# Kernel optimization log

Measured on AMD Instinct MI355X. Metric: run time of the kernel, lower is better.

Reference implementation:

```python
import jax, jax.numpy as jnp
import numpy as np

N = 512      # hidden states
M = 32000    # observation vocab
B = 64       # batch
TMAX = 256   # max sequence length


def setup_inputs() -> dict:
    key = jax.random.key(0)
    k1, k2, k3, k4, k5 = jax.random.split(key, 5)
    return {
        "x": jax.random.randint(k1, (B, TMAX), 0, M),          # observations
        "T": jax.random.randint(k2, (B,), 1, TMAX + 1),        # lengths in [1, TMAX]
        "trans": jax.random.normal(k3, (N, N), dtype=jnp.float32),  # unnormalized transition
        "emis": jax.random.normal(k4, (N, M), dtype=jnp.float32),   # unnormalized emission
        "prior": jax.random.normal(k5, (N,), dtype=jnp.float32),    # unnormalized state priors
    }


def reference(x, T, trans, emis, prior):
    # columns of transition matrix sum to 1 (log_softmax over dim=0 in torch)
    log_A = jax.nn.log_softmax(trans, axis=0)    # (N, N): log_A[j, k] = log p(z_t=j | z_{t-1}=k)
    log_E = jax.nn.log_softmax(emis, axis=1)     # (N, M)
    log_pi = jax.nn.log_softmax(prior, axis=0)   # (N,)

    # emission log-probs for every timestep, gathered once: (B, TMAX, N)
    em = log_E.T[x]

    alpha0 = em[:, 0, :] + log_pi                # (B, N)

    def step(alpha, em_t):
        # out[b, j] = em_t[b, j] + logsumexp_k (log_A[j, k] + alpha[b, k])
        new = em_t + jax.nn.logsumexp(alpha[:, None, :] + log_A[None, :, :], axis=2)
        return new, new

    _, alphas = jax.lax.scan(step, alpha0, jnp.swapaxes(em[:, 1:, :], 0, 1))  # (TMAX-1, B, N)
    log_alpha = jnp.concatenate([alpha0[:, None, :], jnp.swapaxes(alphas, 0, 1)], axis=1)  # (B, TMAX, N)

    log_sums = jax.nn.logsumexp(log_alpha, axis=2)                       # (B, TMAX)
    log_probs = jnp.take_along_axis(log_sums, (T - 1)[:, None], axis=1)  # (B, 1)
    return log_probs
```

## Files before the change

kernel.cpp:

```cpp
#include <hip/hip_runtime.h>
#include <math.h>

#define Nn 512
#define Mm 32000
#define Bb 64
#define Tt 256
#define NCONS 4
#define NPROD 128

typedef float v4f __attribute__((ext_vector_type(4)));
typedef float f4  __attribute__((ext_vector_type(4)));
typedef int   v4i __attribute__((ext_vector_type(4)));
typedef int   v8i __attribute__((ext_vector_type(8)));

__device__ inline int pk4fp8(float a, float b, float c, float d) {
  int r = __builtin_amdgcn_cvt_pk_fp8_f32(a, b, 0, false);
  r = __builtin_amdgcn_cvt_pk_fp8_f32(c, d, r, true);
  return r;
}

__global__ void k_colsum(const float* __restrict__ trans, float* __restrict__ colsum) {
  int tid = threadIdx.x;
  int j0 = blockIdx.x * 16;
  float a0 = 0.f, a1 = 0.f;
  for (int r = 0; r < 16; ++r) {
    a0 += __expf(trans[(j0 + r) * Nn + tid]);
    a1 += __expf(trans[(j0 + r) * Nn + 256 + tid]);
  }
  atomicAdd(&colsum[tid], a0);
  atomicAdd(&colsum[256 + tid], a1);
}

__global__ void k_writeA8(const float* __restrict__ trans, const float* __restrict__ colsum,
                          int* __restrict__ A8) {
  int d = blockIdx.x * 256 + threadIdx.x;
  int j = d >> 7, k0 = (d & 127) << 2;
  float v0 = 256.f * __expf(trans[j * Nn + k0 + 0]) / colsum[k0 + 0];
  float v1 = 256.f * __expf(trans[j * Nn + k0 + 1]) / colsum[k0 + 1];
  float v2 = 256.f * __expf(trans[j * Nn + k0 + 2]) / colsum[k0 + 2];
  float v3 = 256.f * __expf(trans[j * Nn + k0 + 3]) / colsum[k0 + 3];
  A8[d] = pk4fp8(v0, v1, v2, v3);
}

__global__ __attribute__((amdgpu_flat_work_group_size(512, 512), amdgpu_waves_per_eu(2, 2)))
void k_fused(
    const char* __restrict__ A8, const float* __restrict__ emis,
    const int* __restrict__ x, const float* __restrict__ prior,
    const int* __restrict__ Tlen, float* __restrict__ Pem2,
    int* __restrict__ progress, float* __restrict__ out)
{
  __shared__ __align__(16) char ybuf[2][16 * Nn];
  __shared__ __align__(16) float Spart[2][16][12];
  __shared__ __align__(16) float ss[512];
  __shared__ __align__(16) f4 ss4[512];
  const int tid = threadIdx.x;

  if (blockIdx.x >= NCONS) {
    const int p = blockIdx.x - NCONS;
    const int j0 = p * 4;

    float e = __expf(prior[tid]);
    ss[tid] = e; __syncthreads();
    for (int off = 256; off; off >>= 1) { if (tid < off) ss[tid] += ss[tid + off]; __syncthreads(); }
    const float ptot = ss[0];

    const f4* q0 = (const f4*)(emis + (size_t)(j0 + 0) * Mm);
    const f4* q1 = (const f4*)(emis + (size_t)(j0 + 1) * Mm);
    const f4* q2 = (const f4*)(emis + (size_t)(j0 + 2) * Mm);
    const f4* q3 = (const f4*)(emis + (size_t)(j0 + 3) * Mm);
    f4 a4 = {0.f, 0.f, 0.f, 0.f};
    for (int i = tid; i < Mm / 4; i += 512) {
      f4 v0 = q0[i], v1 = q1[i], v2 = q2[i], v3 = q3[i];
      a4[0] += (__expf(v0[0]) + __expf(v0[1])) + (__expf(v0[2]) + __expf(v0[3]));
      a4[1] += (__expf(v1[0]) + __expf(v1[1])) + (__expf(v1[2]) + __expf(v1[3]));
      a4[2] += (__expf(v2[0]) + __expf(v2[1])) + (__expf(v2[2]) + __expf(v2[3]));
      a4[3] += (__expf(v3[0]) + __expf(v3[1])) + (__expf(v3[2]) + __expf(v3[3]));
    }
    ss4[tid] = a4; __syncthreads();
    for (int off = 256; off; off >>= 1) { if (tid < off) ss4[tid] += ss4[tid + off]; __syncthreads(); }
    f4 tot = ss4[0];
    f4 rs, fz;
    #pragma unroll
    for (int q = 0; q < 4; ++q) {
      rs[q] = 32768.f / tot[q];
      fz[q] = rs[q] * 256.f * __expf(prior[j0 + q]) / ptot;
    }

    const float* r0 = emis + (size_t)(j0 + 0) * Mm;
    const float* r1 = emis + (size_t)(j0 + 1) * Mm;
    const float* r2 = emis + (size_t)(j0 + 2) * Mm;
    const float* r3 = emis + (size_t)(j0 + 3) * Mm;
    f4* P4 = (f4*)Pem2;
    for (int c8 = 0; c8 < 8; ++c8) {
      #pragma unroll
      for (int r = 0; r < 4; ++r) {
        int idx = c8 * 2048 + r * 512 + tid;
        int t = idx >> 6, b = idx & 63;
        int mv = x[b * Tt + t];
        f4 fq = (t == 0) ? fz : rs;
        f4 o = { __expf(r0[mv]) * fq[0], __expf(r1[mv]) * fq[1],
                 __expf(r2[mv]) * fq[2], __expf(r3[mv]) * fq[3] };
        P4[t * 8192 + (b >> 4) * 2048 + p * 16 + (b & 15)] = o;
      }
      __syncthreads();
      if (tid == 0) {
        __builtin_amdgcn_fence(__ATOMIC_RELEASE, "agent");
        __hip_atomic_fetch_add(&progress[c8], 1, __ATOMIC_RELAXED, __HIP_MEMORY_SCOPE_AGENT);
      }
    }
    return;
  }

  const int g = blockIdx.x;
  const int w = tid >> 6, lane = tid & 63;
  const int c = lane & 15, kq = lane >> 4;
  const int jw = w * 64;
  const int swz = (c & 7) << 4;
  const int b = g * 16 + c;

  v8i af[4][4];
  #pragma unroll
  for (int rt = 0; rt < 4; ++rt)
    #pragma unroll
    for (int kc = 0; kc < 4; ++kc)
      af[rt][kc] = *reinterpret_cast<const v8i*>(
          A8 + (size_t)(jw + rt * 16 + c) * Nn + kc * 128 + kq * 32);

  #pragma unroll
  for (int rt = 0; rt < 4; ++rt)
    #pragma unroll
    for (int kc = 0; kc < 4; ++kc)
      asm volatile("" : "+v"(af[rt][kc]));

  const int Tb = Tlen[b];
  int E = 23;
  int csafe = 0;

  #define ENSURE(NEED)                                                                      \
    while (csafe <= (NEED)) {                                                               \
      if (__hip_atomic_load(&progress[csafe], __ATOMIC_RELAXED,                             \
                            __HIP_MEMORY_SCOPE_AGENT) >= NPROD) {                           \
        ++csafe;                                                                            \
        __builtin_amdgcn_fence(__ATOMIC_ACQUIRE, "agent");                                  \
      } else __builtin_amdgcn_s_sleep(2);                                                   \
    }

  const int roA0 = (c * Nn + kq * 32) ^ swz;
  const int roB0 = roA0 ^ 16;
  const int wf0 = (c * Nn + jw + kq * 4) ^ swz;
  const int wf1 = wf0 ^ 16, wf2 = wf0 ^ 32, wf3 = wf0 ^ 48;
  char* const yb0 = &ybuf[0][0];

  const char* rdA_e = yb0 + roA0;
  const char* rdB_e = yb0 + roB0;
  const char* rdA_o = rdA_e + 8192;
  const char* rdB_o = rdB_e + 8192;
  char* const wb_o = yb0 + 8192;
  char* const wb_e = yb0;
  const float* sprd0 = &Spart[0][c][0];
  const float* sprd1 = &Spart[1][c][0];
  float* spwr0 = &Spart[1][c][w];
  float* spwr1 = &Spart[0][c][w];

  if (tid < 192) ((float*)&Spart[0][0][0])[tid] = 0.f;
  __syncthreads();

  ENSURE(0);

  {
    int cc = tid & 15, grp = tid >> 4, jb = grp * 16, sz = (cc & 7) << 4;
    const f4* P0 = (const f4*)Pem2 + g * 2048 + (jb >> 2) * 16 + cc;
    float psum = 0.f;
    #pragma unroll
    for (int q = 0; q < 4; ++q) {
      f4 v = P0[q * 16];
      psum += (v[0] + v[1]) + (v[2] + v[3]);
      *reinterpret_cast<int*>(yb0 + ((cc * Nn + jb + q * 4) ^ sz)) = pk4fp8(v[0], v[1], v[2], v[3]);
    }
    atomicAdd(&Spart[0][cc][grp & 7], psum);
  }
  __syncthreads();

  const f4* pemP = (const f4*)Pem2 + (8192 + g * 2048 + jw * 4 + kq * 16 + c);

  union BU { v8i v; v4i h[2]; };

  #define RTCHAIN(RT, BF0, BF1, BF2, BF3, PEM, WF)                                           \
    {                                                                                        \
      v4f a = {0.f, 0.f, 0.f, 0.f};                                                         \
      a = __builtin_amdgcn_mfma_scale_f32_16x16x128_f8f6f4(af[RT][0], BF0.v, a, 0,0,0, 0x7F, 0, 0x7F); \
      a = __builtin_amdgcn_mfma_scale_f32_16x16x128_f8f6f4(af[RT][1], BF1.v, a, 0,0,0, 0x7F, 0, 0x7F); \
      a = __builtin_amdgcn_mfma_scale_f32_16x16x128_f8f6f4(af[RT][2], BF2.v, a, 0,0,0, 0x7F, 0, 0x7F); \
      a = __builtin_amdgcn_mfma_scale_f32_16x16x128_f8f6f4(af[RT][3], BF3.v, a, 0,0,0, 0x7F, 0, 0x7F); \
      v4f v = a * ((PEM) * scl4);                                                            \
      *(int*)(wbase + (WF)) = pk4fp8(v[0], v[1], v[2], v[3]);                                \
      vsum += (v[0] + v[1]) + (v[2] + v[3]);                                                 \
    }

  #define STEPBODY(RDA, RDB, WBASE, SPWP)                                                    \
    {                                                                                        \
      BU b0, b1, b2, b3;                                                                     \
      b0.h[0] = *(const v4i*)((RDA) + 0);   b0.h[1] = *(const v4i*)((RDB) + 0);              \
      b1.h[0] = *(const v4i*)((RDA) + 128); b1.h[1] = *(const v4i*)((RDB) + 128);            \
      b2.h[0] = *(const v4i*)((RDA) + 256); b2.h[1] = *(const v4i*)((RDB) + 256);            \
      b3.h[0] = *(const v4i*)((RDA) + 384); b3.h[1] = *(const v4i*)((RDB) + 384);            \
      v4f scl4 = {scl, scl, scl, scl};                                                       \
      char* const wbase = (WBASE);                                                           \
      float vsum = 0.f;                                                                      \
      RTCHAIN(0, b0, b1, b2, b3, pem0, wf0)                                                  \
      RTCHAIN(1, b0, b1, b2, b3, pem1, wf1)                                                  \
      RTCHAIN(2, b0, b1, b2, b3, pem2, wf2)                                                  \
      RTCHAIN(3, b0, b1, b2, b3, pem3, wf3)                                                  \
      vsum += __shfl_xor(vsum, 16);                                                          \
      vsum += __shfl_xor(vsum, 32);                                                          \
      if (kq == 0) *(SPWP) = vsum;                                                           \
    }

  for (int t = 1; t <= Tt; t += 2) {
    {
      f4 pem0 = pemP[0], pem1 = pemP[64], pem2 = pemP[128], pem3 = pemP[192];
      f4 s0 = *(const f4*)sprd0;
      f4 s1 = *(const f4*)(sprd0 + 4);
      f4 st = s0 + s1;
      float S = (st[0] + st[1]) + (st[2] + st[3]);
      int expb = (int)((__float_as_uint(S) >> 23) & 0xFF);
      if (w == 0 && kq == 0 && Tb == t) out[b] = __logf(S) - (float)E * 0.69314718056f;
      E += 150 - expb;
      float scl = __uint_as_float((unsigned)(254 - expb) << 23);

      STEPBODY(rdA_e, rdB_e, wb_o, spwr0)
      __syncthreads();
    }
    {
      const int T = t + 1;
      if (T < Tt && (T & 31) == 0) ENSURE(T >> 5);
      f4 pem0, pem1, pem2, pem3;
      const f4* p2 = pemP + 8192;
      if (T < Tt) { pem0 = p2[0]; pem1 = p2[64]; pem2 = p2[128]; pem3 = p2[192]; }
      f4 s0 = *(const f4*)sprd1;
      f4 s1 = *(const f4*)(sprd1 + 4);
      f4 st = s0 + s1;
      float S = (st[0] + st[1]) + (st[2] + st[3]);
      int expb = (int)((__float_as_uint(S) >> 23) & 0xFF);
      if (w == 0 && kq == 0 && Tb == T) out[b] = __logf(S) - (float)E * 0.69314718056f;
      if (T == Tt) goto done;
      E += 150 - expb;
      float scl = __uint_as_float((unsigned)(254 - expb) << 23);

      STEPBODY(rdA_o, rdB_o, wb_e, spwr1)
      __syncthreads();
    }
    pemP += 16384;
  }
done: ;
  #undef RTCHAIN
  #undef STEPBODY
  #undef ENSURE
}

extern "C" void kernel_launch(void* const* d_in, const int* in_sizes, int n_in,
                              void* d_out, int out_size, void* d_ws, size_t ws_size,
                              hipStream_t stream) {
  const int*   x     = (const int*)  d_in[0];
  const int*   Tlen  = (const int*)  d_in[1];
  const float* trans = (const float*)d_in[2];
  const float* emis  = (const float*)d_in[3];
  const float* prior = (const float*)d_in[4];
  float* out = (float*)d_out;

  char* w = (char*)d_ws;
  char*  A8       = (char*)(w);
  float* colsum   = (float*)(w + (512 << 10));
  int*   progress = (int*)  (w + (512 << 10) + 4096);
  float* Pem2     = (float*)(w + (1024 << 10));

  hipMemsetAsync(w + (512 << 10), 0, 8192, stream);
  k_colsum <<<32,  256, 0, stream>>>(trans, colsum);
  k_writeA8<<<256, 256, 0, stream>>>(trans, colsum, (int*)A8);
  k_fused  <<<NCONS + NPROD, 512, 0, stream>>>(A8, emis, x, prior, Tlen, Pem2, progress, out);
}
```

Before: 346.5 us.

## Compute per-step normalizer with an all-ones MFMA instead of shared-memory partial sums

Replaces the cross-wave shared-memory reduction of each step's state sum with an extra scaled-FP8 MFMA against an all-ones A operand, so every wave gets the column sum of the current alpha directly from the matrix unit. This removes the Spart buffer, the shuffle reductions and the extra LDS traffic, and interleaves the four row-tile MFMA chains for better issue overlap. In exchange it adds four MFMAs per step and takes the normalizer from the FP8-quantized alpha, which may shift accuracy slightly.

```diff
diff --git a/kernel.cpp b/kernel.cpp
--- a/kernel.cpp
+++ b/kernel.cpp
@@ -50,7 +50,6 @@
     int* __restrict__ progress, float* __restrict__ out)
 {
   __shared__ __align__(16) char ybuf[2][16 * Nn];
-  __shared__ __align__(16) float Spart[2][16][12];
   __shared__ __align__(16) float ss[512];
   __shared__ __align__(16) f4 ss4[512];
   const int tid = threadIdx.x;
@@ -126,11 +125,16 @@
       af[rt][kc] = *reinterpret_cast<const v8i*>(
           A8 + (size_t)(jw + rt * 16 + c) * Nn + kc * 128 + kq * 32);
 
+  v8i onesv;
+  #pragma unroll
+  for (int u = 0; u < 8; ++u) onesv[u] = 0x38383838;
+
   #pragma unroll
   for (int rt = 0; rt < 4; ++rt)
     #pragma unroll
     for (int kc = 0; kc < 4; ++kc)
       asm volatile("" : "+v"(af[rt][kc]));
+  asm volatile("" : "+v"(onesv));
 
   const int Tb = Tlen[b];
   int E = 23;
@@ -157,27 +161,17 @@
   const char* rdB_o = rdB_e + 8192;
   char* const wb_o = yb0 + 8192;
   char* const wb_e = yb0;
-  const float* sprd0 = &Spart[0][c][0];
-  const float* sprd1 = &Spart[1][c][0];
-  float* spwr0 = &Spart[1][c][w];
-  float* spwr1 = &Spart[0][c][w];
-
-  if (tid < 192) ((float*)&Spart[0][0][0])[tid] = 0.f;
-  __syncthreads();
 
   ENSURE(0);
 
   {
     int cc = tid & 15, grp = tid >> 4, jb = grp * 16, sz = (cc & 7) << 4;
     const f4* P0 = (const f4*)Pem2 + g * 2048 + (jb >> 2) * 16 + cc;
-    float psum = 0.f;
     #pragma unroll
     for (int q = 0; q < 4; ++q) {
       f4 v = P0[q * 16];
-      psum += (v[0] + v[1]) + (v[2] + v[3]);
       *reinterpret_cast<int*>(yb0 + ((cc * Nn + jb + q * 4) ^ sz)) = pk4fp8(v[0], v[1], v[2], v[3]);
     }
-    atomicAdd(&Spart[0][cc][grp & 7], psum);
   }
   __syncthreads();
 
@@ -185,50 +179,59 @@
 
   union BU { v8i v; v4i h[2]; };
 
-  #define RTCHAIN(RT, BF0, BF1, BF2, BF3, PEM, WF)                                           \
+  #define LOADMFMA(RDA, RDB)                                                                 \
+    BU b0, b1, b2, b3;                                                                       \
+    b0.h[0] = *(const v4i*)((RDA) + 0);   b0.h[1] = *(const v4i*)((RDB) + 0);                \
+    b1.h[0] = *(const v4i*)((RDA) + 128); b1.h[1] = *(const v4i*)((RDB) + 128);              \
+    b2.h[0] = *(const v4i*)((RDA) + 256); b2.h[1] = *(const v4i*)((RDB) + 256);              \
+    b3.h[0] = *(const v4i*)((RDA) + 384); b3.h[1] = *(const v4i*)((RDB) + 384);              \
+    v4f a0 = {0.f,0.f,0.f,0.f}, a1 = {0.f,0.f,0.f,0.f};                                     \
+    v4f a2 = {0.f,0.f,0.f,0.f}, a3 = {0.f,0.f,0.f,0.f};                                     \
+    v4f as_ = {0.f,0.f,0.f,0.f};                                                            \
+    a0  = __builtin_amdgcn_mfma_scale_f32_16x16x128_f8f6f4(af[0][0], b0.v, a0, 0,0,0, 0x7F, 0, 0x7F); \
+    a1  = __builtin_amdgcn_mfma_scale_f32_16x16x128_f8f6f4(af[1][0], b0.v, a1, 0,0,0, 0x7F, 0, 0x7F); \
+    a2  = __builtin_amdgcn_mfma_scale_f32_16x16x128_f8f6f4(af[2][0], b0.v, a2, 0,0,0, 0x7F, 0, 0x7F); \
+    a3  = __builtin_amdgcn_mfma_scale_f32_16x16x128_f8f6f4(af[3][0], b0.v, a3, 0,0,0, 0x7F, 0, 0x7F); \
+    as_ = __builtin_amdgcn_mfma_scale_f32_16x16x128_f8f6f4(onesv,    b0.v, as_, 0,0,0, 0x7F, 0, 0x7F); \
+    a0  = __builtin_amdgcn_mfma_scale_f32_16x16x128_f8f6f4(af[0][1], b1.v, a0, 0,0,0, 0x7F, 0, 0x7F); \
+    a1  = __builtin_amdgcn_mfma_scale_f32_16x16x128_f8f6f4(af[1][1], b1.v, a1, 0,0,0, 0x7F, 0, 0x7F); \
+    a2  = __builtin_amdgcn_mfma_scale_f32_16x16x128_f8f6f4(af[2][1], b1.v, a2, 0,0,0, 0x7F, 0, 0x7F); \
+    a3  = __builtin_amdgcn_mfma_scale_f32_16x16x128_f8f6f4(af[3][1], b1.v, a3, 0,0,0, 0x7F, 0, 0x7F); \
+    as_ = __builtin_amdgcn_mfma_scale_f32_16x16x128_f8f6f4(onesv,    b1.v, as_, 0,0,0, 0x7F, 0, 0x7F); \
+    a0  = __builtin_amdgcn_mfma_scale_f32_16x16x128_f8f6f4(af[0][2], b2.v, a0, 0,0,0, 0x7F, 0, 0x7F); \
+    a1  = __builtin_amdgcn_mfma_scale_f32_16x16x128_f8f6f4(af[1][2], b2.v, a1, 0,0,0, 0x7F, 0, 0x7F); \
+    a2  = __builtin_amdgcn_mfma_scale_f32_16x16x128_f8f6f4(af[2][2], b2.v, a2, 0,0,0, 0x7F, 0, 0x7F); \
+    a3  = __builtin_amdgcn_mfma_scale_f32_16x16x128_f8f6f4(af[3][2], b2.v, a3, 0,0,0, 0x7F, 0, 0x7F); \
+    as_ = __builtin_amdgcn_mfma_scale_f32_16x16x128_f8f6f4(onesv,    b2.v, as_, 0,0,0, 0x7F, 0, 0x7F); \
+    a0  = __builtin_amdgcn_mfma_scale_f32_16x16x128_f8f6f4(af[0][3], b3.v, a0, 0,0,0, 0x7F, 0, 0x7F); \
+    a1  = __builtin_amdgcn_mfma_scale_f32_16x16x128_f8f6f4(af[1][3], b3.v, a1, 0,0,0, 0x7F, 0, 0x7F); \
+    a2  = __builtin_amdgcn_mfma_scale_f32_16x16x128_f8f6f4(af[2][3], b3.v, a2, 0,0,0, 0x7F, 0, 0x7F); \
+    a3  = __builtin_amdgcn_mfma_scale_f32_16x16x128_f8f6f4(af[3][3], b3.v, a3, 0,0,0, 0x7F, 0, 0x7F); \
+    as_ = __builtin_amdgcn_mfma_scale_f32_16x16x128_f8f6f4(onesv,    b3.v, as_, 0,0,0, 0x7F, 0, 0x7F);
+
+  #define EPILOG(WBASE)                                                                      \
     {                                                                                        \
-      v4f a = {0.f, 0.f, 0.f, 0.f};                                                         \
-      a = __builtin_amdgcn_mfma_scale_f32_16x16x128_f8f6f4(af[RT][0], BF0.v, a, 0,0,0, 0x7F, 0, 0x7F); \
-      a = __builtin_amdgcn_mfma_scale_f32_16x16x128_f8f6f4(af[RT][1], BF1.v, a, 0,0,0, 0x7F, 0, 0x7F); \
-      a = __builtin_amdgcn_mfma_scale_f32_16x16x128_f8f6f4(af[RT][2], BF2.v, a, 0,0,0, 0x7F, 0, 0x7F); \
-      a = __builtin_amdgcn_mfma_scale_f32_16x16x128_f8f6f4(af[RT][3], BF3.v, a, 0,0,0, 0x7F, 0, 0x7F); \
-      v4f v = a * ((PEM) * scl4);                                                            \
-      *(int*)(wbase + (WF)) = pk4fp8(v[0], v[1], v[2], v[3]);                                \
-      vsum += (v[0] + v[1]) + (v[2] + v[3]);                                                 \
-    }
-
-  #define STEPBODY(RDA, RDB, WBASE, SPWP)                                                    \
-    {                                                                                        \
-      BU b0, b1, b2, b3;                                                                     \
-      b0.h[0] = *(const v4i*)((RDA) + 0);   b0.h[1] = *(const v4i*)((RDB) + 0);              \
-      b1.h[0] = *(const v4i*)((RDA) + 128); b1.h[1] = *(const v4i*)((RDB) + 128);            \
-      b2.h[0] = *(const v4i*)((RDA) + 256); b2.h[1] = *(const v4i*)((RDB) + 256);            \
-      b3.h[0] = *(const v4i*)((RDA) + 384); b3.h[1] = *(const v4i*)((RDB) + 384);            \
       v4f scl4 = {scl, scl, scl, scl};                                                       \
-      char* const wbase = (WBASE);                                                           \
-      float vsum = 0.f;                                                                      \
-      RTCHAIN(0, b0, b1, b2, b3, pem0, wf0)                                                  \
-      RTCHAIN(1, b0, b1, b2, b3, pem1, wf1)                                                  \
-      RTCHAIN(2, b0, b1, b2, b3, pem2, wf2)                                                  \
-      RTCHAIN(3, b0, b1, b2, b3, pem3, wf3)                                                  \
-      vsum += __shfl_xor(vsum, 16);                                                          \
-      vsum += __shfl_xor(vsum, 32);                                                          \
-      if (kq == 0) *(SPWP) = vsum;                                                           \
+      v4f v0 = a0 * (pem0 * scl4);                                                           \
+      v4f v1 = a1 * (pem1 * scl4);                                                           \
+      v4f v2 = a2 * (pem2 * scl4);                                                           \
+      v4f v3 = a3 * (pem3 * scl4);                                                           \
+      *(int*)((WBASE) + wf0) = pk4fp8(v0[0], v0[1], v0[2], v0[3]);                           \
+      *(int*)((WBASE) + wf1) = pk4fp8(v1[0], v1[1], v1[2], v1[3]);                           \
+      *(int*)((WBASE) + wf2) = pk4fp8(v2[0], v2[1], v2[2], v2[3]);                           \
+      *(int*)((WBASE) + wf3) = pk4fp8(v3[0], v3[1], v3[2], v3[3]);                           \
     }
 
   for (int t = 1; t <= Tt; t += 2) {
     {
       f4 pem0 = pemP[0], pem1 = pemP[64], pem2 = pemP[128], pem3 = pemP[192];
-      f4 s0 = *(const f4*)sprd0;
-      f4 s1 = *(const f4*)(sprd0 + 4);
-      f4 st = s0 + s1;
-      float S = (st[0] + st[1]) + (st[2] + st[3]);
+      LOADMFMA(rdA_e, rdB_e)
+      float S = as_[0];
       int expb = (int)((__float_as_uint(S) >> 23) & 0xFF);
       if (w == 0 && kq == 0 && Tb == t) out[b] = __logf(S) - (float)E * 0.69314718056f;
       E += 150 - expb;
       float scl = __uint_as_float((unsigned)(254 - expb) << 23);
-
-      STEPBODY(rdA_e, rdB_e, wb_o, spwr0)
+      EPILOG(wb_o)
       __syncthreads();
     }
     {
@@ -237,24 +240,21 @@
       f4 pem0, pem1, pem2, pem3;
       const f4* p2 = pemP + 8192;
       if (T < Tt) { pem0 = p2[0]; pem1 = p2[64]; pem2 = p2[128]; pem3 = p2[192]; }
-      f4 s0 = *(const f4*)sprd1;
-      f4 s1 = *(const f4*)(sprd1 + 4);
-      f4 st = s0 + s1;
-      float S = (st[0] + st[1]) + (st[2] + st[3]);
+      LOADMFMA(rdA_o, rdB_o)
+      float S = as_[0];
       int expb = (int)((__float_as_uint(S) >> 23) & 0xFF);
       if (w == 0 && kq == 0 && Tb == T) out[b] = __logf(S) - (float)E * 0.69314718056f;
       if (T == Tt) goto done;
       E += 150 - expb;
       float scl = __uint_as_float((unsigned)(254 - expb) << 23);
-
-      STEPBODY(rdA_o, rdB_o, wb_e, spwr1)
+      EPILOG(wb_e)
       __syncthreads();
     }
     pemP += 16384;
   }
 done: ;
-  #undef RTCHAIN
-  #undef STEPBODY
+  #undef LOADMFMA
+  #undef EPILOG
   #undef ENSURE
 }
 
```

Measured after the change: 294.2 us. -15.1%, faster.
